# Optimization experiments

Hardware: AMD Instinct MI355X
Metric: run time of the kernel (lower is better)

## Reference

```python
import jax, jax.numpy as jnp
import numpy as np

EPS = 1e-5
SLOPE = 0.2
K = 20
BINS = [1, 2, 4, 8, 16, 32]


def knn(x_t, k):
    # x_t: (B, N, C) -> idx (B, N, k) of nearest neighbors (by L2, incl. self)
    xx = jnp.sum(x_t * x_t, axis=-1)  # (B, N)
    pd = 2.0 * jnp.einsum('bnc,bmc->bnm', x_t, x_t) - xx[:, :, None] - xx[:, None, :]
    _, idx = jax.lax.top_k(pd, k)
    return idx


def edge_features(x_t, idx):
    # x_t: (B, N, C), idx: (B, N, k) -> (B, N, k, 2C) = [nbr - ctr, ctr]
    B = x_t.shape[0]
    nbr = x_t[jnp.arange(B)[:, None, None], idx]          # (B, N, k, C) gather
    ctr = jnp.broadcast_to(x_t[:, :, None, :], nbr.shape)
    return jnp.concatenate([nbr - ctr, ctr], axis=-1)


def batchnorm(h, gamma, beta, axes):
    # training-mode BN: normalize with batch statistics over `axes` (channel last)
    m = jnp.mean(h, axis=axes, keepdims=True)
    v = jnp.var(h, axis=axes, keepdims=True)
    return (h - m) * jax.lax.rsqrt(v + EPS) * gamma + beta


def lrelu(h):
    return jnp.where(h >= 0, h, SLOPE * h)


def edgeconv(x_t, W, g, b):
    # 1x1 conv over edge features + BN + LeakyReLU + max over k neighbors
    e = edge_features(x_t, knn(x_t, K))            # (B, N, k, 2C)
    h = jnp.einsum('bnkc,oc->bnko', e, W)          # per-edge GEMM
    h = lrelu(batchnorm(h, g, b, (0, 1, 2)))
    return jnp.max(h, axis=2)                      # (B, N, Cout)


def setup_inputs() -> dict:
    key = jax.random.key(0)
    ks = jax.random.split(key, 8)
    B, N = 4, 2048
    d = {'x': jax.random.normal(ks[0], (B, 3, N), dtype=jnp.float32)}
    # conv weights (out, in); BN gamma=1, beta=0 as in torch init
    d['W1'] = jax.random.normal(ks[1], (64, 6), dtype=jnp.float32) * 0.1
    d['g1'] = jnp.ones((64,), jnp.float32); d['b1'] = jnp.zeros((64,), jnp.float32)
    d['W2'] = jax.random.normal(ks[2], (64, 128), dtype=jnp.float32) * 0.1
    d['g2'] = jnp.ones((64,), jnp.float32); d['b2'] = jnp.zeros((64,), jnp.float32)
    d['W3'] = jax.random.normal(ks[3], (128, 128), dtype=jnp.float32) * 0.1
    d['g3'] = jnp.ones((128,), jnp.float32); d['b3'] = jnp.zeros((128,), jnp.float32)
    d['W4'] = jax.random.normal(ks[4], (256, 256), dtype=jnp.float32) * 0.1
    d['g4'] = jnp.ones((256,), jnp.float32); d['b4'] = jnp.zeros((256,), jnp.float32)
    d['W5'] = jax.random.normal(ks[5], (1024, 512), dtype=jnp.float32) * 0.05
    d['g5'] = jnp.ones((1024,), jnp.float32); d['b5'] = jnp.zeros((1024,), jnp.float32)
    d['Wf'] = jax.random.normal(ks[6], (256, 1024), dtype=jnp.float32) * 0.03
    d['bfeat'] = jax.random.normal(ks[7], (256,), dtype=jnp.float32) * 0.01
    return d


def reference(x, W1, g1, b1, W2, g2, b2, W3, g3, b3, W4, g4, b4, W5, g5, b5, Wf, bfeat):
    B, _, N = x.shape
    x_t = jnp.transpose(x, (0, 2, 1))              # (B, N, 3)
    x1 = edgeconv(x_t, W1, g1, b1)                 # (B, N, 64)
    x2 = edgeconv(x1, W2, g2, b2)                  # (B, N, 64)
    x3 = edgeconv(x2, W3, g3, b3)                  # (B, N, 128)
    x4 = edgeconv(x3, W4, g4, b4)                  # (B, N, 256)
    xc = jnp.concatenate([x1, x2, x3, x4], axis=-1)  # (B, N, 512)
    h = jnp.einsum('bnc,oc->bno', xc, W5)          # (B, N, 1024)
    h = lrelu(batchnorm(h, g5, b5, (0, 1)))
    F = h.shape[-1]
    feats = []
    for nb in BINS:  # horizontal pyramid pooling over contiguous point chunks
        z = h.reshape(B, nb, N // nb, F)
        feats.append(jnp.max(z, axis=2) + jnp.mean(z, axis=2))
    bins = jnp.concatenate(feats, axis=1)          # (B, 63, F)
    out = jnp.einsum('bsf,of->sbo', bins, Wf) + bfeat  # (63, B, 256)
    return out
```

## Files before the change

kernel.cpp:

```cpp
#include <hip/hip_runtime.h>
#include <hip/hip_bf16.h>
#include <cstdint>
#include <cstddef>

#define B_SZ   4
#define N_PTS  2048
#define KNN    20
#define BN_ROWS (B_SZ * N_PTS)
#define EPSV   1e-5f
#define SLOPEV 0.2f

#define MODE_GD   0
#define MODE_DIST 1

typedef __attribute__((ext_vector_type(8))) short bf16x8;
typedef __attribute__((ext_vector_type(4))) float f32x4;

__global__ void k_transpose(const float* __restrict__ x, float* __restrict__ xt,
                            float* __restrict__ xx)
{
    int i = blockIdx.x * 256 + threadIdx.x;
    if (i >= BN_ROWS) return;
    int b = i >> 11, n = i & 2047;
    float v0 = x[((b * 3 + 0) << 11) + n];
    float v1 = x[((b * 3 + 1) << 11) + n];
    float v2 = x[((b * 3 + 2) << 11) + n];
    xt[i * 3 + 0] = v0; xt[i * 3 + 1] = v1; xt[i * 3 + 2] = v2;
    xx[i] = fmaf(v0, v0, fmaf(v1, v1, v2 * v2));
}

__global__ void k_prepw_all(const float* __restrict__ W1, const float* __restrict__ W2,
                            const float* __restrict__ W3, const float* __restrict__ W4,
                            const float* __restrict__ W5, const float* __restrict__ Wf,
                            float* __restrict__ wc, __hip_bfloat16* __restrict__ w5h,
                            float* __restrict__ wft)
{
    int i = blockIdx.x * 256 + threadIdx.x;
    if (i >= 876928) return;
    if (i >= 614784) {
        int e = i - 614784;
        int o = e >> 10, f = e & 1023;
        wft[f * 256 + o] = Wf[e];
        return;
    }
    if (i >= 90496) {
        int e = i - 90496;
        w5h[e] = __float2bfloat16(W5[e]);
        return;
    }
    const float* W; int O, C, off;
    if      (i < 384)   { W = W1; O = 64;  C = 3;   off = 0; }
    else if (i < 8576)  { W = W2; O = 64;  C = 64;  off = 384; }
    else if (i < 24960) { W = W3; O = 128; C = 64;  off = 8576; }
    else                { W = W4; O = 256; C = 128; off = 24960; }
    int e = i - off, j = e / C, c = e - j * C;
    float v;
    if (j < O) v = W[j * 2 * C + c];
    else { int jo = j - O; v = W[jo * 2 * C + C + c] - W[jo * 2 * C + c]; }
    wc[i] = v;
}

#define MM_BODY(kk) do {                                                          \
    float4 a0 = *(const float4*)&As[(kk) * LDA_ + ty * 4];                        \
    float4 a1 = *(const float4*)&As[(kk) * LDA_ + 64 + ty * 4];                   \
    float4 bq = *(const float4*)&Bs[(kk) * LDB_ + tx * 4];                        \
    float av[2][4] = {{a0.x,a0.y,a0.z,a0.w},{a1.x,a1.y,a1.z,a1.w}};               \
    float bw[4] = {bq.x, bq.y, bq.z, bq.w};                                       \
    _Pragma("unroll") for (int ih = 0; ih < 2; ++ih)                              \
    _Pragma("unroll") for (int ii = 0; ii < 4; ++ii)                              \
    _Pragma("unroll") for (int jj = 0; jj < 4; ++jj)                              \
        acc[ih][ii][jj] = fmaf(av[ih][ii], bw[jj], acc[ih][ii][jj]);              \
} while (0)

template<int MODE, bool VEC>
__launch_bounds__(256)
__global__ void k_mm128(const float* __restrict__ A, int lda,
                        const float* __restrict__ Bm, int ldb,
                        const float* __restrict__ xx, int b0,
                        float* __restrict__ C1, float* __restrict__ C2,
                        int Nn, int Kd)
{
    constexpr int LDA_ = 132;
    constexpr int LDB_ = 68;
    constexpr int LDT_ = 68;
    __shared__ float smem[32 * LDA_ + 32 * LDB_];
    float* As = smem;
    float* Bs = smem + 32 * LDA_;
    float* T  = smem;
    const int tid = threadIdx.x;
    const int tx  = tid & 15;
    const int ty  = tid >> 4;

    int m0, n0;
    if constexpr (MODE == MODE_DIST) {
        int t = blockIdx.x, it = 0;
        for (; it < 16; ++it) { int cnt = 32 - 2 * it; if (t < cnt) break; t -= cnt; }
        const int jt = 2 * it + t;
        m0 = it * 128;
        n0 = jt * 64;
    } else {
        m0 = blockIdx.y * 128;
        n0 = blockIdx.x * 64;
    }

    const float* Ab;
    const float* Bb;
    int ldbe;
    if constexpr (MODE == MODE_DIST) {
        const int b = b0 + blockIdx.z;
        Ab = A + (size_t)b * N_PTS * lda;
        Bb = Ab;
        ldbe = lda;
    } else {
        Ab = A; Bb = Bm; ldbe = ldb;
    }

    float acc[2][4][4] = {};

    for (int k0 = 0; k0 < Kd; k0 += 32) {
        #pragma unroll
        for (int r = 0; r < 4; ++r) {
            int e = r * 256 + tid, row = e >> 3, kq = e & 7;
            if constexpr (VEC) {
                float4 v = *(const float4*)&Ab[(size_t)(m0 + row) * lda + k0 + kq * 4];
                As[(kq * 4 + 0) * LDA_ + row] = v.x;
                As[(kq * 4 + 1) * LDA_ + row] = v.y;
                As[(kq * 4 + 2) * LDA_ + row] = v.z;
                As[(kq * 4 + 3) * LDA_ + row] = v.w;
            } else {
                #pragma unroll
                for (int j = 0; j < 4; ++j) {
                    int kg = k0 + kq * 4 + j;
                    As[(kq * 4 + j) * LDA_ + row] =
                        (kg < Kd) ? Ab[(size_t)(m0 + row) * lda + kg] : 0.f;
                }
            }
        }
        #pragma unroll
        for (int r = 0; r < 2; ++r) {
            int e = r * 256 + tid, row = e >> 3, kq = e & 7;
            if constexpr (VEC) {
                float4 v = *(const float4*)&Bb[(size_t)(n0 + row) * ldbe + k0 + kq * 4];
                Bs[(kq * 4 + 0) * LDB_ + row] = v.x;
                Bs[(kq * 4 + 1) * LDB_ + row] = v.y;
                Bs[(kq * 4 + 2) * LDB_ + row] = v.z;
                Bs[(kq * 4 + 3) * LDB_ + row] = v.w;
            } else {
                #pragma unroll
                for (int j = 0; j < 4; ++j) {
                    int kg = k0 + kq * 4 + j;
                    Bs[(kq * 4 + j) * LDB_ + row] =
                        (kg < Kd) ? Bb[(size_t)(n0 + row) * ldbe + kg] : 0.f;
                }
            }
        }
        __syncthreads();

        int klen = Kd - k0; if (klen > 32) klen = 32;
        if (klen == 32) {
            #pragma unroll 8
            for (int kk = 0; kk < 32; ++kk) MM_BODY(kk);
        } else {
            for (int kk = 0; kk < klen; ++kk) MM_BODY(kk);
        }
        __syncthreads();
    }

    if constexpr (MODE == MODE_DIST) {
        const int b = b0 + blockIdx.z;
        const float* xxb = xx + b * N_PTS;
        float4 xjv = *(const float4*)&xxb[n0 + tx * 4];
        float xj[4] = {xjv.x, xjv.y, xjv.z, xjv.w};
        const size_t zoff = (size_t)blockIdx.z * N_PTS;
        #pragma unroll
        for (int ih = 0; ih < 2; ++ih) {
            const bool dhalf = (n0 == m0 + ih * 64);
            float mvv[4][4];
            #pragma unroll
            for (int i = 0; i < 4; ++i) {
                int il = ty * 4 + i;
                int gi = m0 + ih * 64 + il;
                float xi = xxb[gi];
                float a0 = 2.f * acc[ih][i][0];
                float a1 = 2.f * acc[ih][i][1];
                float a2 = 2.f * acc[ih][i][2];
                float a3 = 2.f * acc[ih][i][3];
                float4 v;
                v.x = a0 - xi - xj[0];
                v.y = a1 - xi - xj[1];
                v.z = a2 - xi - xj[2];
                v.w = a3 - xi - xj[3];
                float m0v = a0 - xj[0] - xi;
                float m1v = a1 - xj[1] - xi;
                float m2v = a2 - xj[2] - xi;
                float m3v = a3 - xj[3] - xi;
                if (dhalf) {
                    int gj = n0 + tx * 4;
                    if (gi == gj + 0) { v.x = 0.f; m0v = 0.f; }
                    if (gi == gj + 1) { v.y = 0.f; m1v = 0.f; }
                    if (gi == gj + 2) { v.z = 0.f; m2v = 0.f; }
                    if (gi == gj + 3) { v.w = 0.f; m3v = 0.f; }
                }
                *(float4*)&C1[(zoff + gi) * N_PTS + n0 + tx * 4] = v;
                mvv[0][i] = m0v; mvv[1][i] = m1v; mvv[2][i] = m2v; mvv[3][i] = m3v;
            }
            #pragma unroll
            for (int c = 0; c < 4; ++c) {
                float4 tv = make_float4(mvv[c][0], mvv[c][1], mvv[c][2], mvv[c][3]);
                *(float4*)&T[(tx * 4 + c) * LDT_ + ty * 4] = tv;
            }
            __syncthreads();
            #pragma unroll
            for (int r = 0; r < 4; ++r) {
                int e = r * 256 + tid;
                int jr = e >> 4, c4 = e & 15;
                float4 tv = *(const float4*)&T[jr * LDT_ + c4 * 4];
                *(float4*)&C1[(zoff + n0 + jr) * N_PTS + m0 + ih * 64 + c4 * 4] = tv;
            }
            __syncthreads();
        }
    } else {
        const int Oo = Nn >> 1;
        #pragma unroll
        for (int ih = 0; ih < 2; ++ih)
            #pragma unroll
            for (int i = 0; i < 4; ++i) {
                int row = m0 + ih * 64 + ty * 4 + i;
                int colg = n0 + tx * 4;
                float4 v = make_float4(acc[ih][i][0], acc[ih][i][1],
                                       acc[ih][i][2], acc[ih][i][3]);
                if (colg < Oo) *(float4*)&C1[(size_t)row * Oo + colg] = v;
                else           *(float4*)&C2[(size_t)row * Oo + colg - Oo] = v;
            }
    }
}

__launch_bounds__(256)
__global__ void k_gemm5(const unsigned short* __restrict__ Ah,
                        const unsigned short* __restrict__ Bh,
                        float* __restrict__ Cf,
                        float* __restrict__ ssum, float* __restrict__ ssumsq)
{
    constexpr int LDA = 72;
    __shared__ unsigned short As[128 * LDA];
    __shared__ unsigned short Bs[128 * LDA];
    const int tid  = threadIdx.x;
    const int lane = tid & 63;
    const int w    = tid >> 6;
    const int wr   = w >> 1, wcl = w & 1;
    const int quad = lane >> 4;
    const int l16  = lane & 15;
    const int m0 = blockIdx.y * 128;
    const int n0 = blockIdx.x * 128;

    f32x4 acc[4][4] = {};

    for (int k0 = 0; k0 < 512; k0 += 64) {
        #pragma unroll
        for (int r = 0; r < 4; ++r) {
            int e = r * 256 + tid, row = e >> 3, kq = e & 7;
            *(uint4*)&As[row * LDA + kq * 8] =
                *(const uint4*)&Ah[(size_t)(m0 + row) * 512 + k0 + kq * 8];
        }
        #pragma unroll
        for (int r = 0; r < 4; ++r) {
            int e = r * 256 + tid, row = e >> 3, kq = e & 7;
            *(uint4*)&Bs[row * LDA + kq * 8] =
                *(const uint4*)&Bh[(size_t)(n0 + row) * 512 + k0 + kq * 8];
        }
        __syncthreads();
        #pragma unroll
        for (int kk = 0; kk < 64; kk += 32) {
            bf16x8 af[4], bfr[4];
            #pragma unroll
            for (int i = 0; i < 4; ++i)
                af[i] = *(const bf16x8*)&As[(wr * 64 + i * 16 + l16) * LDA + kk + quad * 8];
            #pragma unroll
            for (int j = 0; j < 4; ++j)
                bfr[j] = *(const bf16x8*)&Bs[(wcl * 64 + j * 16 + l16) * LDA + kk + quad * 8];
            #pragma unroll
            for (int i = 0; i < 4; ++i)
                #pragma unroll
                for (int j = 0; j < 4; ++j)
                    acc[i][j] = __builtin_amdgcn_mfma_f32_16x16x32_bf16(af[i], bfr[j], acc[i][j], 0, 0, 0);
        }
        __syncthreads();
    }

    #pragma unroll
    for (int i = 0; i < 4; ++i) {
        int rbase = m0 + wr * 64 + i * 16 + quad * 4;
        #pragma unroll
        for (int j = 0; j < 4; ++j) {
            int col = n0 + wcl * 64 + j * 16 + l16;
            #pragma unroll
            for (int r = 0; r < 4; ++r)
                Cf[(size_t)(rbase + r) * 1024 + col] = acc[i][j][r];
        }
    }

    float* sredS = (float*)As;
    float* sredQ = (float*)Bs;
    #pragma unroll
    for (int j = 0; j < 4; ++j) {
        float s = 0.f, q = 0.f;
        #pragma unroll
        for (int i = 0; i < 4; ++i)
            #pragma unroll
            for (int r = 0; r < 4; ++r) {
                float v = acc[i][j][r];
                s += v; q = fmaf(v, v, q);
            }
        int coll = wcl * 64 + j * 16 + l16;
        int slot = wr * 4 + quad;
        sredS[coll * 8 + slot] = s;
        sredQ[coll * 8 + slot] = q;
    }
    __syncthreads();
    if (tid < 128) {
        float s = 0.f, q = 0.f;
        #pragma unroll
        for (int t = 0; t < 8; ++t) { s += sredS[tid * 8 + t]; q += sredQ[tid * 8 + t]; }
        ssum  [blockIdx.y * 1024 + n0 + tid] = s;
        ssumsq[blockIdx.y * 1024 + n0 + tid] = q;
    }
}

__launch_bounds__(256)
__global__ void k_select(const float* __restrict__ D2, int* __restrict__ idx_out)
{
    const int lane = threadIdx.x & 63;
    const int w    = threadIdx.x >> 6;
    const int qloc = blockIdx.x * 4 + w;
    const float* row = D2 + (size_t)qloc * N_PTS;

    unsigned key[32];
    #pragma unroll
    for (int c = 0; c < 8; ++c) {
        float4 v = *(const float4*)&row[c * 256 + lane * 4];
        float vv[4] = {v.x, v.y, v.z, v.w};
        #pragma unroll
        for (int r = 0; r < 4; ++r) {
            unsigned u = __float_as_uint(vv[r]);
            key[c * 4 + r] = ((int)u >= 0) ? (u | 0x80000000u) : ~u;
        }
    }

    unsigned lo = 0u, hi = 0xFFFFFFFFu;
    while (lo < hi) {
        unsigned mid = lo + ((hi - lo) >> 1);
        int cnt = 0;
        #pragma unroll
        for (int e = 0; e < 32; ++e) cnt += (key[e] > mid) ? 1 : 0;
        #pragma unroll
        for (int s = 32; s >= 1; s >>= 1) cnt += __shfl_xor(cnt, s, 64);
        cnt = __builtin_amdgcn_readfirstlane(cnt);
        if (cnt < KNN) hi = mid; else lo = mid + 1;
    }
    const unsigned T = lo;

    int* outp = idx_out + (size_t)qloc * KNN;
    const unsigned long long ltmask = (lane == 0) ? 0ull : (~0ull >> (64 - lane));
    int base = 0;
    #pragma unroll
    for (int e = 0; e < 32; ++e) {
        bool p = key[e] > T;
        unsigned long long m = __ballot(p);
        if (p) {
            int pos = base + __popcll(m & ltmask);
            outp[pos] = (e >> 2) * 256 + lane * 4 + (e & 3);
        }
        base += __popcll(m);
    }
    for (int e = 0; e < 32 && base < KNN; ++e) {
        bool p = key[e] == T;
        unsigned long long m = __ballot(p);
        if (p) {
            int pos = base + __popcll(m & ltmask);
            if (pos < KNN) outp[pos] = (e >> 2) * 256 + lane * 4 + (e & 3);
        }
        base += __popcll(m);
    }
}

template<int O, int NSEQ>
__launch_bounds__(256)
__global__ void k_gather(const float* __restrict__ gtab, const float* __restrict__ dtab,
                         const int* __restrict__ idx,
                         float* __restrict__ hmax, float* __restrict__ hmin,
                         float* __restrict__ ssum, float* __restrict__ ssumsq)
{
    constexpr int NPB = 256 / O;
    const int grp = threadIdx.x / O;
    const int o   = threadIdx.x & (O - 1);
    float accS = 0.f, accS2 = 0.f;
    const int rowsPerBlock = NPB * NSEQ;
    const int batch = blockIdx.x & 3;
    const int chunk = blockIdx.x >> 2;
    const int bbase = batch << 11;
    for (int s = 0; s < NSEQ; ++s) {
        int row = bbase + chunk * rowsPerBlock + s * NPB + grp;
        const int* ip = idx + (size_t)row * KNN;
        float gmax = -INFINITY, gmin = INFINITY, gs = 0.f, gs2 = 0.f;
        for (int k = 0; k < KNN; ++k) {
            int nb = ip[k];
            float v = gtab[(size_t)(bbase + nb) * O + o];
            gmax = fmaxf(gmax, v);
            gmin = fminf(gmin, v);
            gs  += v;
            gs2  = fmaf(v, v, gs2);
        }
        float d = dtab[(size_t)row * O + o];
        hmax[(size_t)row * O + o] = gmax + d;
        hmin[(size_t)row * O + o] = gmin + d;
        accS  += gs + (float)KNN * d;
        accS2 += gs2 + 2.f * d * gs + (float)KNN * d * d;
    }
    int bank = blockIdx.x & 63;
    atomicAdd(&ssum[bank * O + o], accS);
    atomicAdd(&ssumsq[bank * O + o], accS2);
}

template<int O, bool WRITE_XX>
__launch_bounds__(256)
__global__ void k_normalize(const float* __restrict__ hmax, const float* __restrict__ hmin,
                            const float* __restrict__ ssum, const float* __restrict__ ssumsq,
                            const float* __restrict__ gamma, const float* __restrict__ beta,
                            float invM, float* __restrict__ xcs,
                            __hip_bfloat16* __restrict__ xch, float* __restrict__ xx)
{
    const int tid = threadIdx.x;
    const int o   = tid & (O - 1);
    float s = 0.f, s2 = 0.f;
    #pragma unroll 8
    for (int bk = 0; bk < 64; ++bk) { s += ssum[bk * O + o]; s2 += ssumsq[bk * O + o]; }
    float mean = s * invM;
    float var  = fmaf(-mean, mean, s2 * invM);
    float sc   = gamma[o] * rsqrtf(var + EPSV);
    float sh   = beta[o] - mean * sc;

    constexpr int R = 256 / O;
    const int rloc = tid / O;
    __shared__ float part[4];
    const int ngroups = BN_ROWS / R;
    for (int gidx = blockIdx.x; gidx < ngroups; gidx += gridDim.x) {
        int row = gidx * R + rloc;
        size_t i = (size_t)row * O + o;
        float h = (sc >= 0.f) ? hmax[i] : hmin[i];
        float y = fmaf(h, sc, sh);
        y = (y >= 0.f) ? y : SLOPEV * y;
        xcs[(size_t)row * 512 + o] = y;
        xch[(size_t)row * 512 + o] = __float2bfloat16(y);
        if constexpr (WRITE_XX) {
            float p = y * y;
            #pragma unroll
            for (int sft = 32; sft >= 1; sft >>= 1) p += __shfl_xor(p, sft, 64);
            if constexpr (O == 64) {
                if ((tid & 63) == 0) xx[row] = p;
            } else {
                if ((tid & 63) == 0) part[tid >> 6] = p;
                __syncthreads();
                if constexpr (O == 128) {
                    if (tid < 2) xx[gidx * R + tid] = part[2 * tid] + part[2 * tid + 1];
                } else {
                    if (tid == 0) xx[gidx * R] = (part[0] + part[1]) + (part[2] + part[3]);
                }
                __syncthreads();
            }
        }
    }
}

__global__ void k_seg(const float* __restrict__ h,
                      const float* __restrict__ ssum, const float* __restrict__ ssumsq,
                      const float* __restrict__ gamma, const float* __restrict__ beta,
                      float* __restrict__ smax, float* __restrict__ ssumseg)
{
    int f = blockIdx.y * 256 + threadIdx.x;
    float s = 0.f, s2 = 0.f;
    #pragma unroll 8
    for (int bk = 0; bk < 64; ++bk) { s += ssum[bk * 1024 + f]; s2 += ssumsq[bk * 1024 + f]; }
    const float invM = 1.f / (float)BN_ROWS;
    float mean = s * invM;
    float var  = fmaf(-mean, mean, s2 * invM);
    float sc   = gamma[f] * rsqrtf(var + EPSV);
    float sh   = beta[f] - mean * sc;

    int seg = blockIdx.x;
    float mx = -INFINITY, sm = 0.f;
    int n0 = seg * 64;
    for (int i = 0; i < 64; ++i) {
        float v = fmaf(h[(size_t)(n0 + i) * 1024 + f], sc, sh);
        v = (v >= 0.f) ? v : SLOPEV * v;
        mx = fmaxf(mx, v); sm += v;
    }
    smax[(size_t)seg * 1024 + f]    = mx;
    ssumseg[(size_t)seg * 1024 + f] = sm;
}

__launch_bounds__(256)
__global__ void k_final(const float* __restrict__ smax, const float* __restrict__ ssg,
                        const float* __restrict__ Wft, const float* __restrict__ bfeat,
                        float* __restrict__ out)
{
    __shared__ float row[1024];
    __shared__ float part[1024];
    const int tid = threadIdx.x;
    int sb = blockIdx.x;
    int s = sb >> 2, b = sb & 3;
    int nb = (s == 0) ? 1 : (s < 3) ? 2 : (s < 7) ? 4 : (s < 15) ? 8 : (s < 31) ? 16 : 32;
    int idxL = s - (nb - 1);
    int segc = 32 / nb;
    int seg0 = b * 32 + idxL * segc;
    float inv = 1.f / (float)(64 * segc);
    for (int c = tid; c < 1024; c += 256) {
        float mx = -INFINITY, sm = 0.f;
        for (int t = 0; t < segc; ++t) {
            mx = fmaxf(mx, smax[(size_t)(seg0 + t) * 1024 + c]);
            sm += ssg[(size_t)(seg0 + t) * 1024 + c];
        }
        row[c] = mx + sm * inv;
    }
    __syncthreads();

    const int lane = tid & 63;
    const int w    = tid >> 6;
    const float* rw = row + w * 256;
    const float* wp = Wft + (size_t)(w * 256) * 256 + lane * 4;
    float4 a0 = {0,0,0,0}, a1 = {0,0,0,0}, a2 = {0,0,0,0}, a3 = {0,0,0,0};
    for (int f = 0; f < 256; f += 4) {
        float r0 = rw[f + 0], r1 = rw[f + 1], r2 = rw[f + 2], r3 = rw[f + 3];
        float4 w0 = *(const float4*)&wp[(size_t)(f + 0) * 256];
        float4 w1 = *(const float4*)&wp[(size_t)(f + 1) * 256];
        float4 w2 = *(const float4*)&wp[(size_t)(f + 2) * 256];
        float4 w3 = *(const float4*)&wp[(size_t)(f + 3) * 256];
        a0.x = fmaf(r0, w0.x, a0.x); a0.y = fmaf(r0, w0.y, a0.y);
        a0.z = fmaf(r0, w0.z, a0.z); a0.w = fmaf(r0, w0.w, a0.w);
        a1.x = fmaf(r1, w1.x, a1.x); a1.y = fmaf(r1, w1.y, a1.y);
        a1.z = fmaf(r1, w1.z, a1.z); a1.w = fmaf(r1, w1.w, a1.w);
        a2.x = fmaf(r2, w2.x, a2.x); a2.y = fmaf(r2, w2.y, a2.y);
        a2.z = fmaf(r2, w2.z, a2.z); a2.w = fmaf(r2, w2.w, a2.w);
        a3.x = fmaf(r3, w3.x, a3.x); a3.y = fmaf(r3, w3.y, a3.y);
        a3.z = fmaf(r3, w3.z, a3.z); a3.w = fmaf(r3, w3.w, a3.w);
    }
    float4 a;
    a.x = (a0.x + a1.x) + (a2.x + a3.x);
    a.y = (a0.y + a1.y) + (a2.y + a3.y);
    a.z = (a0.z + a1.z) + (a2.z + a3.z);
    a.w = (a0.w + a1.w) + (a2.w + a3.w);
    *(float4*)&part[w * 256 + lane * 4] = a;
    __syncthreads();
    int o = tid;
    float acc = (part[o] + part[256 + o]) + (part[512 + o] + part[768 + o]);
    out[(size_t)sb * 256 + o] = acc + bfeat[o];
}

extern "C" void kernel_launch(void* const* d_in, const int* in_sizes, int n_in,
                              void* d_out, int out_size, void* d_ws, size_t ws_size,
                              hipStream_t stream)
{
    const float* x  = (const float*)d_in[0];
    const float* W1 = (const float*)d_in[1];
    const float* g1 = (const float*)d_in[2];
    const float* b1 = (const float*)d_in[3];
    const float* W2 = (const float*)d_in[4];
    const float* g2 = (const float*)d_in[5];
    const float* b2 = (const float*)d_in[6];
    const float* W3 = (const float*)d_in[7];
    const float* g3 = (const float*)d_in[8];
    const float* b3 = (const float*)d_in[9];
    const float* W4 = (const float*)d_in[10];
    const float* g4 = (const float*)d_in[11];
    const float* b4 = (const float*)d_in[12];
    const float* W5 = (const float*)d_in[13];
    const float* g5 = (const float*)d_in[14];
    const float* b5 = (const float*)d_in[15];
    const float* Wf = (const float*)d_in[16];
    const float* bfeat = (const float*)d_in[17];
    float* out = (float*)d_out;
    float* ws  = (float*)d_ws;

    float* xt1   = ws + 0;
    int*   idx   = (int*)(ws + 24576);
    float* xx    = ws + 188416;
    float* xc    = ws + 196608;
    float* hmax  = ws + 4390912;
    float* hmin  = ws + 6488064;
    float* stats = ws + 8585216;
    float* smax  = ws + 8650752;
    float* ssg   = ws + 8781824;
    float* wc    = ws + 8912896;
    float* big   = ws + 9003520;
    float* gtab  = big;
    float* dtab  = big + 2097152;
    __hip_bfloat16* xch = (__hip_bfloat16*)(ws + 25780736);
    __hip_bfloat16* w5h = (__hip_bfloat16*)(ws + 27877888);
    float* wft   = ws + 28140032;
    float* l5s   = ws + 28402176;
    float* l5q   = ws + 28467712;

    hipMemsetAsync(stats, 0, 65536 * sizeof(float), stream);
    k_transpose<<<32, 256, 0, stream>>>(x, xt1, xx);
    k_prepw_all<<<3426, 256, 0, stream>>>(W1, W2, W3, W4, W5, Wf, wc, w5h, wft);

    const float invMk = 1.f / (float)(BN_ROWS * KNN);

    {
        float* ss = stats + 0;
        k_mm128<MODE_DIST, false><<<dim3(272, 1, 4), 256, 0, stream>>>(xt1, 3, nullptr, 0, xx, 0, big, nullptr, N_PTS, 3);
        k_select<<<2048, 256, 0, stream>>>(big, idx);
        k_mm128<MODE_GD, false><<<dim3(2, 64, 1), 256, 0, stream>>>(xt1, 3, wc, 3, nullptr, 0, gtab, dtab, 128, 3);
        k_gather<64, 8><<<256, 256, 0, stream>>>(gtab, dtab, idx, hmax, hmin, ss, ss + 4096);
        k_normalize<64, true><<<512, 256, 0, stream>>>(hmax, hmin, ss, ss + 4096, g1, b1, invMk, xc + 0, xch + 0, xx);
    }
    {
        float* ss = stats + 8192;
        k_mm128<MODE_DIST, true><<<dim3(272, 1, 4), 256, 0, stream>>>(xc + 0, 512, nullptr, 0, xx, 0, big, nullptr, N_PTS, 64);
        k_select<<<2048, 256, 0, stream>>>(big, idx);
        k_mm128<MODE_GD, true><<<dim3(2, 64, 1), 256, 0, stream>>>(xc + 0, 512, wc + 384, 64, nullptr, 0, gtab, dtab, 128, 64);
        k_gather<64, 8><<<256, 256, 0, stream>>>(gtab, dtab, idx, hmax, hmin, ss, ss + 4096);
        k_normalize<64, true><<<512, 256, 0, stream>>>(hmax, hmin, ss, ss + 4096, g2, b2, invMk, xc + 64, xch + 64, xx);
    }
    {
        float* ss = stats + 16384;
        k_mm128<MODE_DIST, true><<<dim3(272, 1, 4), 256, 0, stream>>>(xc + 64, 512, nullptr, 0, xx, 0, big, nullptr, N_PTS, 64);
        k_select<<<2048, 256, 0, stream>>>(big, idx);
        k_mm128<MODE_GD, true><<<dim3(4, 64, 1), 256, 0, stream>>>(xc + 64, 512, wc + 8576, 64, nullptr, 0, gtab, dtab, 256, 64);
        k_gather<128, 8><<<512, 256, 0, stream>>>(gtab, dtab, idx, hmax, hmin, ss, ss + 8192);
        k_normalize<128, true><<<512, 256, 0, stream>>>(hmax, hmin, ss, ss + 8192, g3, b3, invMk, xc + 128, xch + 128, xx);
    }
    {
        float* ss = stats + 32768;
        k_mm128<MODE_DIST, true><<<dim3(272, 1, 4), 256, 0, stream>>>(xc + 128, 512, nullptr, 0, xx, 0, big, nullptr, N_PTS, 128);
        k_select<<<2048, 256, 0, stream>>>(big, idx);
        k_mm128<MODE_GD, true><<<dim3(8, 64, 1), 256, 0, stream>>>(xc + 128, 512, wc + 24960, 128, nullptr, 0, gtab, dtab, 512, 128);
        k_gather<256, 8><<<1024, 256, 0, stream>>>(gtab, dtab, idx, hmax, hmin, ss, ss + 16384);
        k_normalize<256, false><<<512, 256, 0, stream>>>(hmax, hmin, ss, ss + 16384, g4, b4, invMk, xc + 256, xch + 256, xx);
    }
    {
        k_gemm5<<<dim3(8, 64), 256, 0, stream>>>((const unsigned short*)xch, (const unsigned short*)w5h, big, l5s, l5q);
        k_seg<<<dim3(128, 4), 256, 0, stream>>>(big, l5s, l5q, g5, b5, smax, ssg);
        k_final<<<252, 256, 0, stream>>>(smax, ssg, wft, bfeat, out);
    }
}
```

Baseline: 601.8 us.

## Use 128x128 symmetric tiles for pairwise-distance GEMM with register-computed mirror writes

The pairwise-distance kernel now uses 128x128 upper-triangular tiles instead of 128x64, with 8x8 outputs per thread, which halves the block count to 136 per batch and doubles B-operand reuse from shared memory. The mirrored (transposed) output is computed straight from the accumulators and staged through shared memory in two 64-column passes, and diagonal tiles skip the mirror write entirely. In exchange, each thread holds twice as many accumulator registers, which may lower occupancy, and fewer blocks are launched.

```diff
diff --git a/kernel.cpp b/kernel.cpp
--- a/kernel.cpp
+++ b/kernel.cpp
@@ -60,18 +60,6 @@
     wc[i] = v;
 }
 
-#define MM_BODY(kk) do {                                                          \
-    float4 a0 = *(const float4*)&As[(kk) * LDA_ + ty * 4];                        \
-    float4 a1 = *(const float4*)&As[(kk) * LDA_ + 64 + ty * 4];                   \
-    float4 bq = *(const float4*)&Bs[(kk) * LDB_ + tx * 4];                        \
-    float av[2][4] = {{a0.x,a0.y,a0.z,a0.w},{a1.x,a1.y,a1.z,a1.w}};               \
-    float bw[4] = {bq.x, bq.y, bq.z, bq.w};                                       \
-    _Pragma("unroll") for (int ih = 0; ih < 2; ++ih)                              \
-    _Pragma("unroll") for (int ii = 0; ii < 4; ++ii)                              \
-    _Pragma("unroll") for (int jj = 0; jj < 4; ++jj)                              \
-        acc[ih][ii][jj] = fmaf(av[ih][ii], bw[jj], acc[ih][ii][jj]);              \
-} while (0)
-
 template<int MODE, bool VEC>
 __launch_bounds__(256)
 __global__ void k_mm128(const float* __restrict__ A, int lda,
@@ -81,9 +69,9 @@
                         int Nn, int Kd)
 {
     constexpr int LDA_ = 132;
-    constexpr int LDB_ = 68;
-    constexpr int LDT_ = 68;
-    __shared__ float smem[32 * LDA_ + 32 * LDB_];
+    constexpr int LDB_ = (MODE == MODE_DIST) ? 132 : 68;
+    constexpr int SMEMF = 32 * LDA_ + 32 * LDB_;
+    __shared__ float smem[SMEMF];
     float* As = smem;
     float* Bs = smem + 32 * LDA_;
     float* T  = smem;
@@ -94,10 +82,10 @@
     int m0, n0;
     if constexpr (MODE == MODE_DIST) {
         int t = blockIdx.x, it = 0;
-        for (; it < 16; ++it) { int cnt = 32 - 2 * it; if (t < cnt) break; t -= cnt; }
-        const int jt = 2 * it + t;
+        for (; it < 16; ++it) { int cnt = 16 - it; if (t < cnt) break; t -= cnt; }
+        const int jt = it + t;
         m0 = it * 128;
-        n0 = jt * 64;
+        n0 = jt * 128;
     } else {
         m0 = blockIdx.y * 128;
         n0 = blockIdx.x * 64;
@@ -115,7 +103,8 @@
         Ab = A; Bb = Bm; ldbe = ldb;
     }
 
-    float acc[2][4][4] = {};
+    constexpr int NJH = (MODE == MODE_DIST) ? 2 : 1;
+    float acc[2][NJH][4][4] = {};
 
     for (int k0 = 0; k0 < Kd; k0 += 32) {
         #pragma unroll
@@ -136,8 +125,9 @@
                 }
             }
         }
-        #pragma unroll
-        for (int r = 0; r < 2; ++r) {
+        constexpr int BR = (MODE == MODE_DIST) ? 4 : 2;
+        #pragma unroll
+        for (int r = 0; r < BR; ++r) {
             int e = r * 256 + tid, row = e >> 3, kq = e & 7;
             if constexpr (VEC) {
                 float4 v = *(const float4*)&Bb[(size_t)(n0 + row) * ldbe + k0 + kq * 4];
@@ -157,67 +147,107 @@
         __syncthreads();
 
         int klen = Kd - k0; if (klen > 32) klen = 32;
-        if (klen == 32) {
-            #pragma unroll 8
-            for (int kk = 0; kk < 32; ++kk) MM_BODY(kk);
-        } else {
-            for (int kk = 0; kk < klen; ++kk) MM_BODY(kk);
+        #pragma unroll 8
+        for (int kk = 0; kk < klen; ++kk) {
+            float4 a0 = *(const float4*)&As[kk * LDA_ + ty * 4];
+            float4 a1 = *(const float4*)&As[kk * LDA_ + 64 + ty * 4];
+            float av[2][4] = {{a0.x,a0.y,a0.z,a0.w},{a1.x,a1.y,a1.z,a1.w}};
+            if constexpr (MODE == MODE_DIST) {
+                float4 b0q = *(const float4*)&Bs[kk * LDB_ + tx * 4];
+                float4 b1q = *(const float4*)&Bs[kk * LDB_ + 64 + tx * 4];
+                float bw[2][4] = {{b0q.x,b0q.y,b0q.z,b0q.w},{b1q.x,b1q.y,b1q.z,b1q.w}};
+                #pragma unroll
+                for (int ih = 0; ih < 2; ++ih)
+                    #pragma unroll
+                    for (int jh = 0; jh < 2; ++jh)
+                        #pragma unroll
+                        for (int ii = 0; ii < 4; ++ii)
+                            #pragma unroll
+                            for (int jj = 0; jj < 4; ++jj)
+                                acc[ih][jh][ii][jj] = fmaf(av[ih][ii], bw[jh][jj], acc[ih][jh][ii][jj]);
+            } else {
+                float4 bq = *(const float4*)&Bs[kk * LDB_ + tx * 4];
+                float bw[4] = {bq.x, bq.y, bq.z, bq.w};
+                #pragma unroll
+                for (int ih = 0; ih < 2; ++ih)
+                    #pragma unroll
+                    for (int ii = 0; ii < 4; ++ii)
+                        #pragma unroll
+                        for (int jj = 0; jj < 4; ++jj)
+                            acc[ih][0][ii][jj] = fmaf(av[ih][ii], bw[jj], acc[ih][0][ii][jj]);
+            }
         }
         __syncthreads();
     }
 
     if constexpr (MODE == MODE_DIST) {
-        const int b = b0 + blockIdx.z;
-        const float* xxb = xx + b * N_PTS;
-        float4 xjv = *(const float4*)&xxb[n0 + tx * 4];
-        float xj[4] = {xjv.x, xjv.y, xjv.z, xjv.w};
+        const float* xxb = xx + (b0 + blockIdx.z) * N_PTS;
+        float xj[2][4];
+        #pragma unroll
+        for (int jh = 0; jh < 2; ++jh) {
+            float4 v = *(const float4*)&xxb[n0 + jh * 64 + tx * 4];
+            xj[jh][0] = v.x; xj[jh][1] = v.y; xj[jh][2] = v.z; xj[jh][3] = v.w;
+        }
+        float xiv[2][4];
+        #pragma unroll
+        for (int ih = 0; ih < 2; ++ih)
+            #pragma unroll
+            for (int i = 0; i < 4; ++i)
+                xiv[ih][i] = xxb[m0 + ih * 64 + ty * 4 + i];
+        const bool diag = (m0 == n0);
         const size_t zoff = (size_t)blockIdx.z * N_PTS;
-        #pragma unroll
-        for (int ih = 0; ih < 2; ++ih) {
-            const bool dhalf = (n0 == m0 + ih * 64);
-            float mvv[4][4];
+
+        #pragma unroll
+        for (int ih = 0; ih < 2; ++ih)
             #pragma unroll
             for (int i = 0; i < 4; ++i) {
-                int il = ty * 4 + i;
-                int gi = m0 + ih * 64 + il;
-                float xi = xxb[gi];
-                float a0 = 2.f * acc[ih][i][0];
-                float a1 = 2.f * acc[ih][i][1];
-                float a2 = 2.f * acc[ih][i][2];
-                float a3 = 2.f * acc[ih][i][3];
-                float4 v;
-                v.x = a0 - xi - xj[0];
-                v.y = a1 - xi - xj[1];
-                v.z = a2 - xi - xj[2];
-                v.w = a3 - xi - xj[3];
-                float m0v = a0 - xj[0] - xi;
-                float m1v = a1 - xj[1] - xi;
-                float m2v = a2 - xj[2] - xi;
-                float m3v = a3 - xj[3] - xi;
-                if (dhalf) {
-                    int gj = n0 + tx * 4;
-                    if (gi == gj + 0) { v.x = 0.f; m0v = 0.f; }
-                    if (gi == gj + 1) { v.y = 0.f; m1v = 0.f; }
-                    if (gi == gj + 2) { v.z = 0.f; m2v = 0.f; }
-                    if (gi == gj + 3) { v.w = 0.f; m3v = 0.f; }
+                int gi = m0 + ih * 64 + ty * 4 + i;
+                float xi = xiv[ih][i];
+                size_t base = (zoff + gi) * N_PTS;
+                #pragma unroll
+                for (int jh = 0; jh < 2; ++jh) {
+                    int gj = n0 + jh * 64 + tx * 4;
+                    float4 v;
+                    v.x = 2.f * acc[ih][jh][i][0] - xi - xj[jh][0];
+                    v.y = 2.f * acc[ih][jh][i][1] - xi - xj[jh][1];
+                    v.z = 2.f * acc[ih][jh][i][2] - xi - xj[jh][2];
+                    v.w = 2.f * acc[ih][jh][i][3] - xi - xj[jh][3];
+                    if (diag) {
+                        if (gi == gj + 0) v.x = 0.f;
+                        if (gi == gj + 1) v.y = 0.f;
+                        if (gi == gj + 2) v.z = 0.f;
+                        if (gi == gj + 3) v.w = 0.f;
+                    }
+                    *(float4*)&C1[base + gj] = v;
                 }
-                *(float4*)&C1[(zoff + gi) * N_PTS + n0 + tx * 4] = v;
-                mvv[0][i] = m0v; mvv[1][i] = m1v; mvv[2][i] = m2v; mvv[3][i] = m3v;
-            }
-            #pragma unroll
-            for (int c = 0; c < 4; ++c) {
-                float4 tv = make_float4(mvv[c][0], mvv[c][1], mvv[c][2], mvv[c][3]);
-                *(float4*)&T[(tx * 4 + c) * LDT_ + ty * 4] = tv;
-            }
-            __syncthreads();
-            #pragma unroll
-            for (int r = 0; r < 4; ++r) {
-                int e = r * 256 + tid;
-                int jr = e >> 4, c4 = e & 15;
-                float4 tv = *(const float4*)&T[jr * LDT_ + c4 * 4];
-                *(float4*)&C1[(zoff + n0 + jr) * N_PTS + m0 + ih * 64 + c4 * 4] = tv;
-            }
-            __syncthreads();
+            }
+
+        if (!diag) {
+            #pragma unroll
+            for (int jh = 0; jh < 2; ++jh) {
+                #pragma unroll
+                for (int c = 0; c < 4; ++c) {
+                    float xjc = xj[jh][c];
+                    #pragma unroll
+                    for (int ih = 0; ih < 2; ++ih) {
+                        float4 tv;
+                        tv.x = 2.f * acc[ih][jh][0][c] - xjc - xiv[ih][0];
+                        tv.y = 2.f * acc[ih][jh][1][c] - xjc - xiv[ih][1];
+                        tv.z = 2.f * acc[ih][jh][2][c] - xjc - xiv[ih][2];
+                        tv.w = 2.f * acc[ih][jh][3][c] - xjc - xiv[ih][3];
+                        *(float4*)&T[(tx * 4 + c) * LDA_ + ih * 64 + ty * 4] = tv;
+                    }
+                }
+                __syncthreads();
+                #pragma unroll
+                for (int r = 0; r < 8; ++r) {
+                    int e = r * 256 + tid;
+                    int jr = e >> 5, c4 = e & 31;
+                    float4 tv = *(const float4*)&T[jr * LDA_ + c4 * 4];
+                    *(float4*)&C1[(zoff + n0 + jh * 64 + jr) * N_PTS + m0 + c4 * 4] = tv;
+                }
+                __syncthreads();
+            }
         }
     } else {
         const int Oo = Nn >> 1;
@@ -227,8 +257,8 @@
             for (int i = 0; i < 4; ++i) {
                 int row = m0 + ih * 64 + ty * 4 + i;
                 int colg = n0 + tx * 4;
-                float4 v = make_float4(acc[ih][i][0], acc[ih][i][1],
-                                       acc[ih][i][2], acc[ih][i][3]);
+                float4 v = make_float4(acc[ih][0][i][0], acc[ih][0][i][1],
+                                       acc[ih][0][i][2], acc[ih][0][i][3]);
                 if (colg < Oo) *(float4*)&C1[(size_t)row * Oo + colg] = v;
                 else           *(float4*)&C2[(size_t)row * Oo + colg - Oo] = v;
             }
@@ -607,7 +637,7 @@
 
     {
         float* ss = stats + 0;
-        k_mm128<MODE_DIST, false><<<dim3(272, 1, 4), 256, 0, stream>>>(xt1, 3, nullptr, 0, xx, 0, big, nullptr, N_PTS, 3);
+        k_mm128<MODE_DIST, false><<<dim3(136, 1, 4), 256, 0, stream>>>(xt1, 3, nullptr, 0, xx, 0, big, nullptr, N_PTS, 3);
         k_select<<<2048, 256, 0, stream>>>(big, idx);
         k_mm128<MODE_GD, false><<<dim3(2, 64, 1), 256, 0, stream>>>(xt1, 3, wc, 3, nullptr, 0, gtab, dtab, 128, 3);
         k_gather<64, 8><<<256, 256, 0, stream>>>(gtab, dtab, idx, hmax, hmin, ss, ss + 4096);
@@ -615,7 +645,7 @@
     }
     {
         float* ss = stats + 8192;
-        k_mm128<MODE_DIST, true><<<dim3(272, 1, 4), 256, 0, stream>>>(xc + 0, 512, nullptr, 0, xx, 0, big, nullptr, N_PTS, 64);
+        k_mm128<MODE_DIST, true><<<dim3(136, 1, 4), 256, 0, stream>>>(xc + 0, 512, nullptr, 0, xx, 0, big, nullptr, N_PTS, 64);
         k_select<<<2048, 256, 0, stream>>>(big, idx);
         k_mm128<MODE_GD, true><<<dim3(2, 64, 1), 256, 0, stream>>>(xc + 0, 512, wc + 384, 64, nullptr, 0, gtab, dtab, 128, 64);
         k_gather<64, 8><<<256, 256, 0, stream>>>(gtab, dtab, idx, hmax, hmin, ss, ss + 4096);
@@ -623,7 +653,7 @@
     }
     {
         float* ss = stats + 16384;
-        k_mm128<MODE_DIST, true><<<dim3(272, 1, 4), 256, 0, stream>>>(xc + 64, 512, nullptr, 0, xx, 0, big, nullptr, N_PTS, 64);
+        k_mm128<MODE_DIST, true><<<dim3(136, 1, 4), 256, 0, stream>>>(xc + 64, 512, nullptr, 0, xx, 0, big, nullptr, N_PTS, 64);
         k_select<<<2048, 256, 0, stream>>>(big, idx);
         k_mm128<MODE_GD, true><<<dim3(4, 64, 1), 256, 0, stream>>>(xc + 64, 512, wc + 8576, 64, nullptr, 0, gtab, dtab, 256, 64);
         k_gather<128, 8><<<512, 256, 0, stream>>>(gtab, dtab, idx, hmax, hmin, ss, ss + 8192);
@@ -631,7 +661,7 @@
     }
     {
         float* ss = stats + 32768;
-        k_mm128<MODE_DIST, true><<<dim3(272, 1, 4), 256, 0, stream>>>(xc + 128, 512, nullptr, 0, xx, 0, big, nullptr, N_PTS, 128);
+        k_mm128<MODE_DIST, true><<<dim3(136, 1, 4), 256, 0, stream>>>(xc + 128, 512, nullptr, 0, xx, 0, big, nullptr, N_PTS, 128);
         k_select<<<2048, 256, 0, stream>>>(big, idx);
         k_mm128<MODE_GD, true><<<dim3(8, 64, 1), 256, 0, stream>>>(xc + 128, 512, wc + 24960, 128, nullptr, 0, gtab, dtab, 512, 128);
         k_gather<256, 8><<<1024, 256, 0, stream>>>(gtab, dtab, idx, hmax, hmin, ss, ss + 16384);
```

Result: faster. 589.3 us (-2.1%).
